# Optimization experiments

Measured on AMD Instinct MI355X. Metric: run time of the kernel, lower is better.

## Reference

```python
import jax, jax.numpy as jnp
import numpy as np

NUM_NODES = 50000
NUM_EDGES = 800000
DIM = 128


def setup_inputs() -> dict:
    key = jax.random.key(0)
    k0, k1, k2, k3 = jax.random.split(key, 4)
    edge_index = jax.random.randint(k0, (2, NUM_EDGES), 0, NUM_NODES, dtype=jnp.int64)
    emb = jax.random.normal(k1, (NUM_NODES, DIM), dtype=jnp.float32) * 0.02
    s = 1.0 / np.sqrt(DIM)
    W1 = jax.random.normal(k2, (DIM, DIM), dtype=jnp.float32) * s
    b1 = jnp.zeros((DIM,), dtype=jnp.float32)
    W2 = jax.random.normal(k3, (DIM, DIM), dtype=jnp.float32) * s
    b2 = jnp.zeros((DIM,), dtype=jnp.float32)
    return {"edge_index": edge_index, "emb": emb, "W1": W1, "b1": b1, "W2": W2, "b2": b2}


def gcn_conv(x, W, b, src, dst, num_nodes):
    # PyG GCNConv: h = x @ W; out = D^{-1/2}(A+I)D^{-1/2} h + b
    h = x @ W  # [N, D]
    deg = jnp.zeros((num_nodes,), h.dtype).at[dst].add(1.0) + 1.0  # +1 self-loop
    dis = jax.lax.rsqrt(deg)  # deg >= 1 always
    msg = h[src] * (dis[src] * dis[dst])[:, None]  # [E, D]
    agg = jax.ops.segment_sum(msg, dst, num_segments=num_nodes)
    agg = agg + h * (dis * dis)[:, None]  # self-loop term: norm = 1/deg
    return agg + b


def reference(edge_index, emb, W1, b1, W2, b2):
    src, dst = edge_index[0], edge_index[1]
    x = gcn_conv(emb, W1, b1, src, dst, NUM_NODES)
    x = jax.nn.relu(x)
    x = gcn_conv(x, W2, b2, src, dst, NUM_NODES)
    return x
```

## Files before the change

### kernel.cpp

```cpp
#include <hip/hip_runtime.h>
#include <hip/hip_fp16.h>

#define DIM 128
#define SEG 64
#define CAP 60

typedef _Float16 half8 __attribute__((ext_vector_type(8)));
typedef float floatx4 __attribute__((ext_vector_type(4)));


__global__ __launch_bounds__(256) void k_init(unsigned short* __restrict__ csr, int N) {
    int i = blockIdx.x * 256 + threadIdx.x;
    int gs = gridDim.x * 256;
    const uint4 ff = make_uint4(~0u, ~0u, ~0u, ~0u);
    const uint4 head = make_uint4(0u, 0u, ~0u, ~0u);
    int total = N * 8;
    for (int j = i; j < total; j += gs)
        ((uint4*)csr)[j] = ((j & 7) == 0) ? head : ff;
}


__global__ __launch_bounds__(256) void k_fill(const int* __restrict__ ei,
                                              unsigned short* __restrict__ csr,
                                              int E, int N) {
    int e = blockIdx.x * 256 + threadIdx.x;
    if (e < E) {
        int sv = ei[e];
        int dv = ei[E + e];
        if ((unsigned)sv < (unsigned)N && (unsigned)dv < (unsigned)N) {
            int pos = atomicAdd((int*)(csr + (size_t)dv * SEG), 1);
            if (pos < CAP) csr[(size_t)dv * SEG + 4 + pos] = (unsigned short)sv;
        }
    }
}


__global__ __launch_bounds__(256) void k_prep(const unsigned short* __restrict__ csr,
                                              float* __restrict__ dis, int N) {
    int i = blockIdx.x * 256 + threadIdx.x;
    if (i < N) {
        int cnt = *(const int*)(csr + (size_t)i * SEG);
        dis[i] = rsqrtf((float)cnt + 1.0f);
    }
}


__global__ __launch_bounds__(256) void k_packW(const float* __restrict__ W1,
                                               const float* __restrict__ W2,
                                               _Float16* __restrict__ Wp) {
    int gid = blockIdx.x * 256 + threadIdx.x;
    int sel = gid >> 14;
    int flat = gid & 16383;
    int f = flat >> 9;
    int rest = flat & 511;
    int lane = rest >> 3, j = rest & 7;
    int t = f >> 2, s = f & 3;
    int k = s * 32 + (lane >> 4) * 8 + j;
    int n = t * 16 + (lane & 15);
    const float* W = sel ? W2 : W1;
    Wp[(size_t)sel * 16384 + flat] = (_Float16)W[k * DIM + n];
}


template <typename T>
__global__ __launch_bounds__(256) void k_gemm_mfma(const T* __restrict__ X,
                                                   const _Float16* __restrict__ Wp,
                                                   const float* __restrict__ dis,
                                                   __half* __restrict__ out, int N) {
    __shared__ _Float16 ls[64 * 136];
    int tid = threadIdx.x;
    int w = tid >> 6, lane = tid & 63;
    int m = lane & 15, q = lane >> 4;
    int row0 = blockIdx.x * 64 + w * 16;

    int arow = row0 + m;
    bool okA = arow < N;
    half8 a[4];
#pragma unroll
    for (int s = 0; s < 4; ++s) {
        if (okA) {
            if constexpr (sizeof(T) == 2) {
                a[s] = *(const half8*)((const _Float16*)X + (size_t)arow * DIM + s * 32 + q * 8);
            } else {
                const float* Xa = (const float*)X + (size_t)arow * DIM + s * 32 + q * 8;
                float4 f0 = *(const float4*)Xa;
                float4 f1 = *(const float4*)(Xa + 4);
                half8 h;
                h[0] = (_Float16)f0.x; h[1] = (_Float16)f0.y;
                h[2] = (_Float16)f0.z; h[3] = (_Float16)f0.w;
                h[4] = (_Float16)f1.x; h[5] = (_Float16)f1.y;
                h[6] = (_Float16)f1.z; h[7] = (_Float16)f1.w;
                a[s] = h;
            }
        } else {
            a[s] = (half8)(_Float16)0.0f;
        }
    }
    int drow = row0 + q * 4;
    float4 dv = (drow < N) ? *(const float4*)(dis + drow) : make_float4(0.f, 0.f, 0.f, 0.f);
    float dd[4] = {dv.x, dv.y, dv.z, dv.w};

    _Float16* lrow = ls + w * 16 * 136;
#pragma unroll
    for (int t = 0; t < 8; ++t) {
        floatx4 acc = {0.f, 0.f, 0.f, 0.f};
#pragma unroll
        for (int s = 0; s < 4; ++s) {
            half8 b = *(const half8*)(Wp + ((size_t)(t * 4 + s) * 64 + lane) * 8);
            acc = __builtin_amdgcn_mfma_f32_16x16x32_f16(a[s], b, acc, 0, 0, 0);
        }
#pragma unroll
        for (int r = 0; r < 4; ++r)
            lrow[(q * 4 + r) * 136 + t * 16 + m] = (_Float16)(acc[r] * dd[r]);
    }
    __syncthreads();

    int rr = lane >> 2, cc = (lane & 3) * 32;
    int grow = row0 + rr;
    if (grow < N) {
        const uint4* lsrc = (const uint4*)(lrow + rr * 136 + cc);
        uint4* gdst = (uint4*)((__half*)out + (size_t)grow * DIM + cc);
        gdst[0] = lsrc[0];
        gdst[1] = lsrc[1];
        gdst[2] = lsrc[2];
        gdst[3] = lsrc[3];
    }
}


__global__ __launch_bounds__(256) void k_agg(const __half* __restrict__ hn,
                                             const unsigned short* __restrict__ csr,
                                             const float* __restrict__ dis,
                                             const float* __restrict__ bias,
                                             float* __restrict__ outf,
                                             __half* __restrict__ outh,
                                             int N, int do_relu, int nslots) {
    int tid = threadIdx.x;
    int slot0 = (blockIdx.x * 256 + tid) >> 4;
    int c8 = (tid & 15) << 3;

    float4 bv0 = *(const float4*)(bias + c8);
    float4 bv1 = *(const float4*)(bias + c8 + 4);
    float bb[8] = {bv0.x, bv0.y, bv0.z, bv0.w, bv1.x, bv1.y, bv1.z, bv1.w};
    const uint4 z4 = make_uint4(0u, 0u, 0u, 0u);
    const ushort4 sent = make_ushort4(0xFFFFu, 0xFFFFu, 0xFFFFu, 0xFFFFu);

    for (int node = slot0; node < N; node += nslots) {
        const unsigned short* seg = csr + (size_t)node * SEG;
        int cnt = *(const int*)seg;
        uint4 selfv = *(const uint4*)(hn + (size_t)node * DIM + c8);
        float sc = dis[node];
        int pcnt = (cnt + 3) & ~3;
        if (pcnt > CAP) pcnt = CAP;
        const unsigned short* slots = seg + 4;

        float acc[8];
#pragma unroll
        for (int j = 0; j < 8; ++j) acc[j] = 0.f;

        ushort4 ss = (pcnt > 0) ? *(const ushort4*)slots : sent;
        for (int e0 = 0; e0 < pcnt; e0 += 4) {
            ushort4 ssn = (e0 + 4 < pcnt) ? *(const ushort4*)(slots + e0 + 4) : sent;
            uint4 v0 = (ss.x != 0xFFFFu) ? *(const uint4*)(hn + (size_t)ss.x * DIM + c8) : z4;
            uint4 v1 = (ss.y != 0xFFFFu) ? *(const uint4*)(hn + (size_t)ss.y * DIM + c8) : z4;
            uint4 v2 = (ss.z != 0xFFFFu) ? *(const uint4*)(hn + (size_t)ss.z * DIM + c8) : z4;
            uint4 v3 = (ss.w != 0xFFFFu) ? *(const uint4*)(hn + (size_t)ss.w * DIM + c8) : z4;
            const __half2* h0 = (const __half2*)&v0;
            const __half2* h1 = (const __half2*)&v1;
            const __half2* h2 = (const __half2*)&v2;
            const __half2* h3 = (const __half2*)&v3;
#pragma unroll
            for (int j = 0; j < 4; ++j) {
                float2 f0 = __half22float2(h0[j]);
                float2 f1 = __half22float2(h1[j]);
                float2 f2 = __half22float2(h2[j]);
                float2 f3 = __half22float2(h3[j]);
                acc[2 * j]     += (f0.x + f1.x) + (f2.x + f3.x);
                acc[2 * j + 1] += (f0.y + f1.y) + (f2.y + f3.y);
            }
            ss = ssn;
        }

        const __half2* hs = (const __half2*)&selfv;
        float o[8];
#pragma unroll
        for (int j = 0; j < 4; ++j) {
            float2 fs = __half22float2(hs[j]);
            o[2 * j]     = (acc[2 * j]     + fs.x) * sc + bb[2 * j];
            o[2 * j + 1] = (acc[2 * j + 1] + fs.y) * sc + bb[2 * j + 1];
        }
        if (do_relu) {
            __half2 p0 = __floats2half2_rn(fmaxf(o[0], 0.f), fmaxf(o[1], 0.f));
            __half2 p1 = __floats2half2_rn(fmaxf(o[2], 0.f), fmaxf(o[3], 0.f));
            __half2 p2 = __floats2half2_rn(fmaxf(o[4], 0.f), fmaxf(o[5], 0.f));
            __half2 p3 = __floats2half2_rn(fmaxf(o[6], 0.f), fmaxf(o[7], 0.f));
            union { __half2 h[4]; uint4 u; } pu;
            pu.h[0] = p0; pu.h[1] = p1; pu.h[2] = p2; pu.h[3] = p3;
            *(uint4*)(outh + (size_t)node * DIM + c8) = pu.u;
        } else {
            *(float4*)(outf + (size_t)node * DIM + c8) = make_float4(o[0], o[1], o[2], o[3]);
            *(float4*)(outf + (size_t)node * DIM + c8 + 4) = make_float4(o[4], o[5], o[6], o[7]);
        }
    }
}


extern "C" void kernel_launch(void* const* d_in, const int* in_sizes, int n_in,
                              void* d_out, int out_size, void* d_ws, size_t ws_size,
                              hipStream_t stream) {
    const int* ei = (const int*)d_in[0];
    const float* emb = (const float*)d_in[1];
    const float* W1 = (const float*)d_in[2];
    const float* b1 = (const float*)d_in[3];
    const float* W2 = (const float*)d_in[4];
    const float* b2 = (const float*)d_in[5];
    float* out = (float*)d_out;

    int E = in_sizes[0] / 2;
    int N = in_sizes[1] / DIM;

    char* p = (char*)d_ws;
    auto alloc = [&](size_t bytes) -> char* {
        char* r = p;
        p += (bytes + 255) & ~(size_t)255;
        return r;
    };
    unsigned short* csr = (unsigned short*)alloc((size_t)N * SEG * 2);
    float* dis          = (float*)alloc((size_t)N * 4);
    __half* hn          = (__half*)alloc((size_t)N * DIM * 2);
    __half* x2          = (__half*)alloc((size_t)N * DIM * 2);
    _Float16* Wp        = (_Float16*)alloc(2 * 16384 * 2);

    k_init<<<1024, 256, 0, stream>>>(csr, N);
    k_packW<<<128, 256, 0, stream>>>(W1, W2, Wp);
    k_fill<<<(E + 255) / 256, 256, 0, stream>>>(ei, csr, E, N);
    k_prep<<<(N + 255) / 256, 256, 0, stream>>>(csr, dis, N);

    const int AGG_BLOCKS = 3072;
    const int NSLOTS = AGG_BLOCKS * 16;
    const int GB = (N + 63) / 64;

    k_gemm_mfma<float><<<GB, 256, 0, stream>>>(emb, Wp, dis, hn, N);
    k_agg<<<AGG_BLOCKS, 256, 0, stream>>>(hn, csr, dis, b1, nullptr, x2, N, 1, NSLOTS);

    k_gemm_mfma<__half><<<GB, 256, 0, stream>>>(x2, Wp + 16384, dis, hn, N);
    k_agg<<<AGG_BLOCKS, 256, 0, stream>>>(hn, csr, dis, b2, out, nullptr, N, 0, NSLOTS);
}
```

Baseline: 280.8 us.

## Fuse layer-1 aggregation with layer-2 GEMM and fold small kernels

Fuses the layer-1 aggregation, ReLU and layer-2 MFMA GEMM into one kernel that stages 16 aggregated rows in LDS, so the intermediate fp16 activation is never written to and re-read from global memory. The weight packing is merged into the CSR init kernel, and the degree-normalisation kernel is dropped by recomputing rsqrt from the CSR counts wherever it is needed. Aggregation moves from a persistent grid-stride loop to one node per 16-thread group with grid sized to N, cutting launch count from 8 to 5. In exchange, each fused block does a small GEMM reading the full W2 tile per 16 rows, and adds barrier and LDS overhead.

```diff
diff --git a/kernel.cpp b/kernel.cpp
--- a/kernel.cpp
+++ b/kernel.cpp
@@ -9,14 +9,29 @@
 typedef float floatx4 __attribute__((ext_vector_type(4)));
 
 
-__global__ __launch_bounds__(256) void k_init(unsigned short* __restrict__ csr, int N) {
+__global__ __launch_bounds__(256) void k_init_pack(unsigned short* __restrict__ csr, int N,
+                                                   const float* __restrict__ W1,
+                                                   const float* __restrict__ W2,
+                                                   _Float16* __restrict__ Wp) {
     int i = blockIdx.x * 256 + threadIdx.x;
     int gs = gridDim.x * 256;
+    if (i < 32768) {
+        int sel = i >> 14;
+        int flat = i & 16383;
+        int f = flat >> 9;
+        int rest = flat & 511;
+        int lane = rest >> 3, j = rest & 7;
+        int t = f >> 2, s = f & 3;
+        int k = s * 32 + (lane >> 4) * 8 + j;
+        int n = t * 16 + (lane & 15);
+        const float* W = sel ? W2 : W1;
+        Wp[(size_t)sel * 16384 + flat] = (_Float16)W[k * DIM + n];
+    }
     const uint4 ff = make_uint4(~0u, ~0u, ~0u, ~0u);
     const uint4 head = make_uint4(0u, 0u, ~0u, ~0u);
     int total = N * 8;
-    for (int j = i; j < total; j += gs)
-        ((uint4*)csr)[j] = ((j & 7) == 0) ? head : ff;
+    for (int j2 = i; j2 < total; j2 += gs)
+        ((uint4*)csr)[j2] = ((j2 & 7) == 0) ? head : ff;
 }
 
 
@@ -35,38 +50,10 @@
 }
 
 
-__global__ __launch_bounds__(256) void k_prep(const unsigned short* __restrict__ csr,
-                                              float* __restrict__ dis, int N) {
-    int i = blockIdx.x * 256 + threadIdx.x;
-    if (i < N) {
-        int cnt = *(const int*)(csr + (size_t)i * SEG);
-        dis[i] = rsqrtf((float)cnt + 1.0f);
-    }
-}
-
-
-__global__ __launch_bounds__(256) void k_packW(const float* __restrict__ W1,
-                                               const float* __restrict__ W2,
-                                               _Float16* __restrict__ Wp) {
-    int gid = blockIdx.x * 256 + threadIdx.x;
-    int sel = gid >> 14;
-    int flat = gid & 16383;
-    int f = flat >> 9;
-    int rest = flat & 511;
-    int lane = rest >> 3, j = rest & 7;
-    int t = f >> 2, s = f & 3;
-    int k = s * 32 + (lane >> 4) * 8 + j;
-    int n = t * 16 + (lane & 15);
-    const float* W = sel ? W2 : W1;
-    Wp[(size_t)sel * 16384 + flat] = (_Float16)W[k * DIM + n];
-}
-
-
-template <typename T>
-__global__ __launch_bounds__(256) void k_gemm_mfma(const T* __restrict__ X,
-                                                   const _Float16* __restrict__ Wp,
-                                                   const float* __restrict__ dis,
-                                                   __half* __restrict__ out, int N) {
+__global__ __launch_bounds__(256) void k_gemm1(const float* __restrict__ X,
+                                               const unsigned short* __restrict__ csr,
+                                               const _Float16* __restrict__ Wp,
+                                               __half* __restrict__ out, int N) {
     __shared__ _Float16 ls[64 * 136];
     int tid = threadIdx.x;
     int w = tid >> 6, lane = tid & 63;
@@ -79,26 +66,27 @@
 #pragma unroll
     for (int s = 0; s < 4; ++s) {
         if (okA) {
-            if constexpr (sizeof(T) == 2) {
-                a[s] = *(const half8*)((const _Float16*)X + (size_t)arow * DIM + s * 32 + q * 8);
-            } else {
-                const float* Xa = (const float*)X + (size_t)arow * DIM + s * 32 + q * 8;
-                float4 f0 = *(const float4*)Xa;
-                float4 f1 = *(const float4*)(Xa + 4);
-                half8 h;
-                h[0] = (_Float16)f0.x; h[1] = (_Float16)f0.y;
-                h[2] = (_Float16)f0.z; h[3] = (_Float16)f0.w;
-                h[4] = (_Float16)f1.x; h[5] = (_Float16)f1.y;
-                h[6] = (_Float16)f1.z; h[7] = (_Float16)f1.w;
-                a[s] = h;
-            }
+            const float* Xa = X + (size_t)arow * DIM + s * 32 + q * 8;
+            float4 f0 = *(const float4*)Xa;
+            float4 f1 = *(const float4*)(Xa + 4);
+            half8 h;
+            h[0] = (_Float16)f0.x; h[1] = (_Float16)f0.y;
+            h[2] = (_Float16)f0.z; h[3] = (_Float16)f0.w;
+            h[4] = (_Float16)f1.x; h[5] = (_Float16)f1.y;
+            h[6] = (_Float16)f1.z; h[7] = (_Float16)f1.w;
+            a[s] = h;
         } else {
             a[s] = (half8)(_Float16)0.0f;
         }
     }
     int drow = row0 + q * 4;
-    float4 dv = (drow < N) ? *(const float4*)(dis + drow) : make_float4(0.f, 0.f, 0.f, 0.f);
-    float dd[4] = {dv.x, dv.y, dv.z, dv.w};
+    float dd[4];
+#pragma unroll
+    for (int r = 0; r < 4; ++r) {
+        int rr2 = drow + r;
+        int c = (rr2 < N) ? *(const int*)(csr + (size_t)rr2 * SEG) : 0;
+        dd[r] = rsqrtf((float)c + 1.0f);
+    }
 
     _Float16* lrow = ls + w * 16 * 136;
 #pragma unroll
@@ -128,15 +116,17 @@
 }
 
 
-__global__ __launch_bounds__(256) void k_agg(const __half* __restrict__ hn,
-                                             const unsigned short* __restrict__ csr,
-                                             const float* __restrict__ dis,
-                                             const float* __restrict__ bias,
-                                             float* __restrict__ outf,
-                                             __half* __restrict__ outh,
-                                             int N, int do_relu, int nslots) {
+__global__ __launch_bounds__(256) void k_aggemm(const __half* __restrict__ hn,
+                                                const unsigned short* __restrict__ csr,
+                                                const float* __restrict__ bias,
+                                                const _Float16* __restrict__ Wp2,
+                                                __half* __restrict__ hn2, int N) {
+    __shared__ __align__(16) _Float16 As[16 * 136];
+    __shared__ __align__(16) _Float16 Os[16 * 136];
+    __shared__ float sdis[16];
     int tid = threadIdx.x;
-    int slot0 = (blockIdx.x * 256 + tid) >> 4;
+    int slot = tid >> 4;
+    int node = blockIdx.x * 16 + slot;
     int c8 = (tid & 15) << 3;
 
     float4 bv0 = *(const float4*)(bias + c8);
@@ -145,11 +135,14 @@
     const uint4 z4 = make_uint4(0u, 0u, 0u, 0u);
     const ushort4 sent = make_ushort4(0xFFFFu, 0xFFFFu, 0xFFFFu, 0xFFFFu);
 
-    for (int node = slot0; node < N; node += nslots) {
+    union { __half2 h[4]; uint4 u; } pu;
+    pu.u = make_uint4(0u, 0u, 0u, 0u);
+    float sc = 0.f;
+    if (node < N) {
         const unsigned short* seg = csr + (size_t)node * SEG;
         int cnt = *(const int*)seg;
         uint4 selfv = *(const uint4*)(hn + (size_t)node * DIM + c8);
-        float sc = dis[node];
+        sc = rsqrtf((float)cnt + 1.0f);
         int pcnt = (cnt + 3) & ~3;
         if (pcnt > CAP) pcnt = CAP;
         const unsigned short* slots = seg + 4;
@@ -189,19 +182,108 @@
             o[2 * j]     = (acc[2 * j]     + fs.x) * sc + bb[2 * j];
             o[2 * j + 1] = (acc[2 * j + 1] + fs.y) * sc + bb[2 * j + 1];
         }
-        if (do_relu) {
-            __half2 p0 = __floats2half2_rn(fmaxf(o[0], 0.f), fmaxf(o[1], 0.f));
-            __half2 p1 = __floats2half2_rn(fmaxf(o[2], 0.f), fmaxf(o[3], 0.f));
-            __half2 p2 = __floats2half2_rn(fmaxf(o[4], 0.f), fmaxf(o[5], 0.f));
-            __half2 p3 = __floats2half2_rn(fmaxf(o[6], 0.f), fmaxf(o[7], 0.f));
-            union { __half2 h[4]; uint4 u; } pu;
-            pu.h[0] = p0; pu.h[1] = p1; pu.h[2] = p2; pu.h[3] = p3;
-            *(uint4*)(outh + (size_t)node * DIM + c8) = pu.u;
-        } else {
-            *(float4*)(outf + (size_t)node * DIM + c8) = make_float4(o[0], o[1], o[2], o[3]);
-            *(float4*)(outf + (size_t)node * DIM + c8 + 4) = make_float4(o[4], o[5], o[6], o[7]);
-        }
-    }
+        pu.h[0] = __floats2half2_rn(fmaxf(o[0], 0.f), fmaxf(o[1], 0.f));
+        pu.h[1] = __floats2half2_rn(fmaxf(o[2], 0.f), fmaxf(o[3], 0.f));
+        pu.h[2] = __floats2half2_rn(fmaxf(o[4], 0.f), fmaxf(o[5], 0.f));
+        pu.h[3] = __floats2half2_rn(fmaxf(o[6], 0.f), fmaxf(o[7], 0.f));
+    }
+    *(uint4*)((char*)As + slot * 272 + (tid & 15) * 16) = pu.u;
+    if ((tid & 15) == 0) sdis[slot] = sc;
+    __syncthreads();
+
+    int w = tid >> 6, lane = tid & 63;
+    int m = lane & 15, q = lane >> 4;
+    half8 a[4];
+#pragma unroll
+    for (int s = 0; s < 4; ++s)
+        a[s] = *(const half8*)((const char*)As + m * 272 + s * 64 + q * 16);
+    float dd[4];
+#pragma unroll
+    for (int r = 0; r < 4; ++r) dd[r] = sdis[q * 4 + r];
+
+#pragma unroll
+    for (int ti = 0; ti < 2; ++ti) {
+        int t = w * 2 + ti;
+        floatx4 acc2 = {0.f, 0.f, 0.f, 0.f};
+#pragma unroll
+        for (int s = 0; s < 4; ++s) {
+            half8 b = *(const half8*)(Wp2 + ((size_t)(t * 4 + s) * 64 + lane) * 8);
+            acc2 = __builtin_amdgcn_mfma_f32_16x16x32_f16(a[s], b, acc2, 0, 0, 0);
+        }
+#pragma unroll
+        for (int r = 0; r < 4; ++r)
+            Os[(q * 4 + r) * 136 + t * 16 + m] = (_Float16)(acc2[r] * dd[r]);
+    }
+    __syncthreads();
+
+    int rr3 = tid >> 4, ci = tid & 15;
+    int grow = blockIdx.x * 16 + rr3;
+    if (grow < N)
+        *(uint4*)((__half*)hn2 + (size_t)grow * DIM + ci * 8) =
+            *(const uint4*)((const char*)Os + rr3 * 272 + ci * 16);
+}
+
+
+__global__ __launch_bounds__(256) void k_agg_out(const __half* __restrict__ hn,
+                                                 const unsigned short* __restrict__ csr,
+                                                 const float* __restrict__ bias,
+                                                 float* __restrict__ outf, int N) {
+    int tid = threadIdx.x;
+    int node = (blockIdx.x * 256 + tid) >> 4;
+    int c8 = (tid & 15) << 3;
+    if (node >= N) return;
+
+    float4 bv0 = *(const float4*)(bias + c8);
+    float4 bv1 = *(const float4*)(bias + c8 + 4);
+    float bb[8] = {bv0.x, bv0.y, bv0.z, bv0.w, bv1.x, bv1.y, bv1.z, bv1.w};
+    const uint4 z4 = make_uint4(0u, 0u, 0u, 0u);
+    const ushort4 sent = make_ushort4(0xFFFFu, 0xFFFFu, 0xFFFFu, 0xFFFFu);
+
+    const unsigned short* seg = csr + (size_t)node * SEG;
+    int cnt = *(const int*)seg;
+    uint4 selfv = *(const uint4*)(hn + (size_t)node * DIM + c8);
+    float sc = rsqrtf((float)cnt + 1.0f);
+    int pcnt = (cnt + 3) & ~3;
+    if (pcnt > CAP) pcnt = CAP;
+    const unsigned short* slots = seg + 4;
+
+    float acc[8];
+#pragma unroll
+    for (int j = 0; j < 8; ++j) acc[j] = 0.f;
+
+    ushort4 ss = (pcnt > 0) ? *(const ushort4*)slots : sent;
+    for (int e0 = 0; e0 < pcnt; e0 += 4) {
+        ushort4 ssn = (e0 + 4 < pcnt) ? *(const ushort4*)(slots + e0 + 4) : sent;
+        uint4 v0 = (ss.x != 0xFFFFu) ? *(const uint4*)(hn + (size_t)ss.x * DIM + c8) : z4;
+        uint4 v1 = (ss.y != 0xFFFFu) ? *(const uint4*)(hn + (size_t)ss.y * DIM + c8) : z4;
+        uint4 v2 = (ss.z != 0xFFFFu) ? *(const uint4*)(hn + (size_t)ss.z * DIM + c8) : z4;
+        uint4 v3 = (ss.w != 0xFFFFu) ? *(const uint4*)(hn + (size_t)ss.w * DIM + c8) : z4;
+        const __half2* h0 = (const __half2*)&v0;
+        const __half2* h1 = (const __half2*)&v1;
+        const __half2* h2 = (const __half2*)&v2;
+        const __half2* h3 = (const __half2*)&v3;
+#pragma unroll
+        for (int j = 0; j < 4; ++j) {
+            float2 f0 = __half22float2(h0[j]);
+            float2 f1 = __half22float2(h1[j]);
+            float2 f2 = __half22float2(h2[j]);
+            float2 f3 = __half22float2(h3[j]);
+            acc[2 * j]     += (f0.x + f1.x) + (f2.x + f3.x);
+            acc[2 * j + 1] += (f0.y + f1.y) + (f2.y + f3.y);
+        }
+        ss = ssn;
+    }
+
+    const __half2* hs = (const __half2*)&selfv;
+    float o[8];
+#pragma unroll
+    for (int j = 0; j < 4; ++j) {
+        float2 fs = __half22float2(hs[j]);
+        o[2 * j]     = (acc[2 * j]     + fs.x) * sc + bb[2 * j];
+        o[2 * j + 1] = (acc[2 * j + 1] + fs.y) * sc + bb[2 * j + 1];
+    }
+    *(float4*)(outf + (size_t)node * DIM + c8) = make_float4(o[0], o[1], o[2], o[3]);
+    *(float4*)(outf + (size_t)node * DIM + c8 + 4) = make_float4(o[4], o[5], o[6], o[7]);
 }
 
 
@@ -226,23 +308,16 @@
         return r;
     };
     unsigned short* csr = (unsigned short*)alloc((size_t)N * SEG * 2);
-    float* dis          = (float*)alloc((size_t)N * 4);
-    __half* hn          = (__half*)alloc((size_t)N * DIM * 2);
-    __half* x2          = (__half*)alloc((size_t)N * DIM * 2);
+    __half* hn1         = (__half*)alloc((size_t)N * DIM * 2);
+    __half* hn2         = (__half*)alloc((size_t)N * DIM * 2);
     _Float16* Wp        = (_Float16*)alloc(2 * 16384 * 2);
 
-    k_init<<<1024, 256, 0, stream>>>(csr, N);
-    k_packW<<<128, 256, 0, stream>>>(W1, W2, Wp);
+    const int GB = (N + 63) / 64;
+    const int AB = (N + 15) / 16;
+
+    k_init_pack<<<1024, 256, 0, stream>>>(csr, N, W1, W2, Wp);
     k_fill<<<(E + 255) / 256, 256, 0, stream>>>(ei, csr, E, N);
-    k_prep<<<(N + 255) / 256, 256, 0, stream>>>(csr, dis, N);
-
-    const int AGG_BLOCKS = 3072;
-    const int NSLOTS = AGG_BLOCKS * 16;
-    const int GB = (N + 63) / 64;
-
-    k_gemm_mfma<float><<<GB, 256, 0, stream>>>(emb, Wp, dis, hn, N);
-    k_agg<<<AGG_BLOCKS, 256, 0, stream>>>(hn, csr, dis, b1, nullptr, x2, N, 1, NSLOTS);
-
-    k_gemm_mfma<__half><<<GB, 256, 0, stream>>>(x2, Wp + 16384, dis, hn, N);
-    k_agg<<<AGG_BLOCKS, 256, 0, stream>>>(hn, csr, dis, b2, out, nullptr, N, 0, NSLOTS);
-}
+    k_gemm1<<<GB, 256, 0, stream>>>(emb, csr, Wp, hn1, N);
+    k_aggemm<<<AB, 256, 0, stream>>>(hn1, csr, b1, Wp + 16384, hn2, N);
+    k_agg_out<<<AB, 256, 0, stream>>>(hn2, csr, b2, out, N);
+}
```

After: 263.9 us (median of 2 runs). -6.0%, faster.
